# Kernel tuning notes

Measured on AMD Instinct MI355X. Metric: run time of the kernel, lower is better.

The kernel has to match this reference:

```python
import jax, jax.numpy as jnp
import numpy as np

B, S, HID, NH = 2, 2048, 1024, 16
HD = HID // NH  # head_dim = 64


def setup_inputs() -> dict:
    key = jax.random.key(0)
    ks = jax.random.split(key, 9)
    init = 0.02
    return {
        "x": jax.random.normal(ks[0], (B, S, HID), dtype=jnp.float32),
        "Wq": jax.random.normal(ks[1], (HID, HID), dtype=jnp.float32) * init,
        "bq": jnp.zeros((HID,), dtype=jnp.float32),
        "Wk": jax.random.normal(ks[2], (HID, HID), dtype=jnp.float32) * init,
        "bk": jnp.zeros((HID,), dtype=jnp.float32),
        "Wv": jax.random.normal(ks[3], (HID, HID), dtype=jnp.float32) * init,
        "bv": jnp.zeros((HID,), dtype=jnp.float32),
        "Wo": jax.random.normal(ks[4], (HID, HID), dtype=jnp.float32) * init,
        "bo": jnp.zeros((HID,), dtype=jnp.float32),
    }


def _split_heads(t):
    # [B, S, HID] -> [B, NH, S, HD]
    return t.reshape(B, S, NH, HD).transpose(0, 2, 1, 3)


def reference(x, Wq, bq, Wk, bk, Wv, bv, Wo, bo):
    q = _split_heads(x @ Wq.T + bq)
    k = _split_heads(x @ Wk.T + bk)
    v = _split_heads(x @ Wv.T + bv)

    # Faithful to source: scores = QK^T / (head_dim ** -0.5) == QK^T * sqrt(head_dim)
    inv_scale = jnp.asarray(HD ** (-0.5), dtype=x.dtype)
    scores = jnp.einsum("bhqd,bhkd->bhqk", q, k) / inv_scale

    causal_mask = jnp.triu(jnp.ones((S, S), dtype=bool), k=1)  # True above diagonal
    scores = jnp.where(causal_mask, jnp.asarray(-jnp.inf, dtype=scores.dtype), scores)
    attn = jax.nn.softmax(scores, axis=-1)  # dropout = identity (eval mode)

    ctx = jnp.einsum("bhqk,bhkd->bhqd", attn, v)
    ctx = ctx.transpose(0, 2, 1, 3).reshape(B, S, HID)
    out = ctx @ Wo.T + bo  # out_layer Linear; dropout = identity
    return out, attn
```

## Files before the change

kernel.cpp:

```cpp
#include <hip/hip_runtime.h>
#include <hip/hip_bf16.h>

#define BB   2
#define SS   2048
#define HID  1024
#define NH   16
#define HD   64
#define NEGS -30000.0f

typedef __bf16 bf16x8 __attribute__((ext_vector_type(8)));
typedef __bf16 bf16x4 __attribute__((ext_vector_type(4)));
typedef float  f32x4  __attribute__((ext_vector_type(4)));

static __device__ __forceinline__ f32x4 mfma_bf16(bf16x8 a, bf16x8 b, f32x4 c) {
    return __builtin_amdgcn_mfma_f32_16x16x32_bf16(a, b, c, 0, 0, 0);
}

static __device__ __forceinline__ void split_bf16(float f, __bf16* hp, __bf16* lp) {
    __bf16 h = (__bf16)f;
    *hp = h;
    *lp = (__bf16)(f - (float)h);
}

static __device__ __forceinline__ float clampf(float v, float lo, float hi) {
    return fminf(fmaxf(v, lo), hi);
}

static __device__ __forceinline__ void gll16(const __bf16* g, __bf16* l) {
    __builtin_amdgcn_global_load_lds((const void*)g, (void*)l, 16, 0, 0);
}

static __device__ __forceinline__ void barrier_lds() {
    asm volatile("s_waitcnt lgkmcnt(0)" ::: "memory");
    __builtin_amdgcn_sched_barrier(0);
    __builtin_amdgcn_s_barrier();
    __builtin_amdgcn_sched_barrier(0);
}

__global__ __launch_bounds__(256) void split_kernel(
    const float* __restrict__ x,
    const float* __restrict__ Wq, const float* __restrict__ Wk,
    const float* __restrict__ Wv, const float* __restrict__ Wo,
    __bf16* __restrict__ xh, __bf16* __restrict__ xl,
    __bf16* __restrict__ wqh, __bf16* __restrict__ wql,
    __bf16* __restrict__ wkh, __bf16* __restrict__ wkl,
    __bf16* __restrict__ wvh, __bf16* __restrict__ woh)
{
    const int bid = blockIdx.x;
    if (bid < 4096) {
        const int i4 = bid * 256 + threadIdx.x;
        const float4 v = ((const float4*)x)[i4];
        const float* p = (const float*)&v;
        bf16x4 h4, l4v;
#pragma unroll
        for (int j = 0; j < 4; j++) { __bf16 hh, ll; split_bf16(p[j], &hh, &ll); h4[j] = hh; l4v[j] = ll; }
        *(bf16x4*)&xh[(size_t)i4 * 4] = h4;
        *(bf16x4*)&xl[(size_t)i4 * 4] = l4v;
        return;
    }
    const int wb = bid - 4096;
    const int which = (wb >> 10) + 1;
    const int i4 = (wb & 1023) * 256 + threadIdx.x;
    const float* src = which == 1 ? Wq : which == 2 ? Wk : which == 3 ? Wv : Wo;
    const float sc = (which == 1) ? 8.0f : 1.0f;
    const float4 v = ((const float4*)src)[i4];
    const float* p = (const float*)&v;
    bf16x4 h4, l4v;
#pragma unroll
    for (int j = 0; j < 4; j++) { __bf16 hh, ll; split_bf16(p[j] * sc, &hh, &ll); h4[j] = hh; l4v[j] = ll; }
    if (which == 1)      { *(bf16x4*)&wqh[(size_t)i4 * 4] = h4; *(bf16x4*)&wql[(size_t)i4 * 4] = l4v; }
    else if (which == 2) { *(bf16x4*)&wkh[(size_t)i4 * 4] = h4; *(bf16x4*)&wkl[(size_t)i4 * 4] = l4v; }
    else if (which == 3) { *(bf16x4*)&wvh[(size_t)i4 * 4] = h4; }
    else                 { *(bf16x4*)&woh[(size_t)i4 * 4] = h4; }
}

__global__ __launch_bounds__(256) void qkv_kernel(
    const __bf16* __restrict__ xh, const __bf16* __restrict__ xl,
    const __bf16* __restrict__ wqh, const __bf16* __restrict__ wql,
    const __bf16* __restrict__ wkh, const __bf16* __restrict__ wkl,
    const __bf16* __restrict__ wvh,
    const float* __restrict__ bq, const float* __restrict__ bk, const float* __restrict__ bv,
    __bf16* __restrict__ qh, __bf16* __restrict__ ql,
    __bf16* __restrict__ kh, __bf16* __restrict__ kl,
    __bf16* __restrict__ vt)
{
    __shared__ __align__(16) __bf16 smem[32768];

    const int stream = blockIdx.x >> 3, ct = blockIdx.x & 7;
    const int t0 = blockIdx.y * 128, c0 = ct * 128;
    const bool qk = stream < 2;
    const __bf16* const Bhg = stream == 0 ? wqh : stream == 1 ? wkh : wvh;
    const __bf16* const Blg = stream == 0 ? wql : wkl;
    const float* const bias = stream == 0 ? bq : stream == 1 ? bk : bv;
    const float bscale = stream == 0 ? 8.0f : 1.0f;

    const int tid = threadIdx.x, wave = tid >> 6, lane = tid & 63;
    const int l16 = lane & 15, quad = lane >> 4;
    const int wr = wave >> 1, wc = wave & 1;

    const int ar0 = tid >> 2,         as0 = (tid & 3) ^ (ar0 & 3);
    const int ar1 = (256 + tid) >> 2, as1 = ((256 + tid) & 3) ^ (ar1 & 3);
    const size_t aoff0 = (size_t)(t0 + ar0) * HID + as0 * 8;
    const size_t aoff1 = (size_t)(t0 + ar1) * HID + as1 * 8;
    const size_t boff0 = (size_t)(c0 + ar0) * HID + as0 * 8;
    const size_t boff1 = (size_t)(c0 + ar1) * HID + as1 * 8;
    const int ld0 = wave << 9, ld1 = (4 + wave) << 9;

#define QKV_STAGE(b_, k0_) do {                                   \
        __bf16* s_ = smem + (b_) * 16384;                         \
        gll16(xh + aoff0 + (k0_), s_ + ld0);                      \
        gll16(xh + aoff1 + (k0_), s_ + ld1);                      \
        gll16(Bhg + boff0 + (k0_), s_ + 8192 + ld0);              \
        gll16(Bhg + boff1 + (k0_), s_ + 8192 + ld1);              \
        if (qk) {                                                 \
            gll16(xl + aoff0 + (k0_), s_ + 4096 + ld0);           \
            gll16(xl + aoff1 + (k0_), s_ + 4096 + ld1);           \
            gll16(Blg + boff0 + (k0_), s_ + 12288 + ld0);         \
            gll16(Blg + boff1 + (k0_), s_ + 12288 + ld1);         \
        }                                                         \
    } while (0)

    const f32x4 zero4 = {0.f, 0.f, 0.f, 0.f};
    f32x4 acc[4][4];
#pragma unroll
    for (int i = 0; i < 4; i++)
#pragma unroll
        for (int j = 0; j < 4; j++) acc[i][j] = zero4;

    QKV_STAGE(0, 0);
    for (int k0 = 0; k0 < HID; k0 += 32) {
        const int cur = (k0 >> 5) & 1;
        __syncthreads();
        if (k0 + 32 < HID) QKV_STAGE(cur ^ 1, k0 + 32);
        __bf16* const s_ = smem + cur * 16384;

        bf16x8 aH[4], aL[4], bHf[4], bLf[4];
#pragma unroll
        for (int mf = 0; mf < 4; mf++) {
            const int row = wr * 64 + mf * 16 + l16;
            const int off = row * 32 + ((quad ^ (row & 3)) << 3);
            aH[mf] = *(const bf16x8*)(s_ + off);
            if (qk) aL[mf] = *(const bf16x8*)(s_ + 4096 + off);
        }
#pragma unroll
        for (int nf = 0; nf < 4; nf++) {
            const int row = wc * 64 + nf * 16 + l16;
            const int off = row * 32 + ((quad ^ (row & 3)) << 3);
            bHf[nf] = *(const bf16x8*)(s_ + 8192 + off);
            if (qk) bLf[nf] = *(const bf16x8*)(s_ + 12288 + off);
        }
#pragma unroll
        for (int mf = 0; mf < 4; mf++)
#pragma unroll
            for (int nf = 0; nf < 4; nf++) {
                acc[mf][nf] = mfma_bf16(aH[mf], bHf[nf], acc[mf][nf]);
                if (qk) {
                    acc[mf][nf] = mfma_bf16(aH[mf], bLf[nf], acc[mf][nf]);
                    acc[mf][nf] = mfma_bf16(aL[mf], bHf[nf], acc[mf][nf]);
                }
            }
    }
#undef QKV_STAGE

    const int bidx = t0 >> 11;
    const int s0 = t0 & (SS - 1);

    if (qk) {
        __bf16* const Es = smem;
        __bf16* const hi_arr = stream == 0 ? qh : kh;
        __bf16* const lo_arr = stream == 0 ? ql : kl;
#pragma unroll
        for (int pass = 0; pass < 2; pass++) {
            __syncthreads();
#pragma unroll
            for (int nf = 0; nf < 4; nf++) {
                const int dcl = wc * 64 + nf * 16 + l16;
                const float bv_ = bias[c0 + dcl] * bscale;
#pragma unroll
                for (int mf = 0; mf < 4; mf++)
#pragma unroll
                    for (int r = 0; r < 4; r++) {
                        const int srl = wr * 64 + mf * 16 + quad * 4 + r;
                        const float v = clampf(acc[mf][nf][r] + bv_, -1e4f, 1e4f);
                        __bf16 hv, lv;
                        split_bf16(v, &hv, &lv);
                        Es[srl * 132 + dcl] = pass ? lv : hv;
                    }
            }
            __syncthreads();
            __bf16* const dst = pass ? lo_arr : hi_arr;
#pragma unroll
            for (int i = 0; i < 8; i++) {
                const int idx = tid + i * 256;
                const int row = idx >> 4, c16 = idx & 15;
                const int hh = (c0 >> 6) + (c16 >> 3);
                const int dd = (c16 & 7) * 8;
                const size_t o = ((size_t)(bidx * NH + hh) * SS + (s0 + row)) * HD + dd;
                *(uint4*)&dst[o] = *(const uint4*)&Es[row * 132 + c16 * 8];
            }
        }
    } else {
        __syncthreads();
        __bf16* const Vts = smem + wave * 4608;
#pragma unroll
        for (int nf = 0; nf < 4; nf++) {
            const int dloc = nf * 16 + l16;
            const float bv_ = bias[c0 + wc * 64 + dloc];
#pragma unroll
            for (int mf = 0; mf < 4; mf++)
#pragma unroll
                for (int r = 0; r < 4; r++)
                    Vts[dloc * 72 + mf * 16 + quad * 4 + r] =
                        (__bf16)clampf(acc[mf][nf][r] + bv_, -1e4f, 1e4f);
        }
        const int hh = (c0 + wc * 64) >> 6;
        const size_t vb = (size_t)(bidx * NH + hh) * HD * SS;
        const int sc0 = s0 + wr * 64;
#pragma unroll
        for (int j = 0; j < 8; j++) {
            const int idx = j * 64 + lane;
            const int d = idx >> 3, c8 = idx & 7;
            *(uint4*)&vt[vb + (size_t)d * SS + sc0 + c8 * 8] =
                *(const uint4*)&Vts[d * 72 + c8 * 8];
        }
    }
}

__global__ __launch_bounds__(512) void attn_kernel(
    const __bf16* __restrict__ qh, const __bf16* __restrict__ ql,
    const __bf16* __restrict__ kh, const __bf16* __restrict__ kl,
    const __bf16* __restrict__ vt,
    float* __restrict__ attn, __bf16* __restrict__ ctx)
{
    __shared__ __align__(16) __bf16 Kh0[4096], Kl0[4096], Kh1[4096], Kl1[4096];
    __shared__ __align__(16) __bf16 Vt0[4096], Vt1[4096];
    __shared__ __align__(16) __bf16 Ps[128][72];
    __shared__ __align__(16) __bf16 _occ_pad[8192];

    const int bid = blockIdx.x;
    const int g   = bid & 7;
    const int ii  = bid >> 3;
    const int bh  = g + 8 * (ii & 3);
    const int p   = ii >> 2;
    const int b   = bh >> 4, h = bh & 15;

    const int tid  = threadIdx.x;
    const int wave = tid >> 6, lane = tid & 63;
    const int l16  = lane & 15, quad = lane >> 4;

    const int sr = tid >> 3, ssw = (tid & 7) ^ (sr & 7);
    const size_t kq = (size_t)sr * HD + ssw * 8;
    const size_t vq = (size_t)sr * SS + ssw * 8;
    const int ldw = wave << 9;

    const __bf16* const khp = kh + (size_t)bh * SS * HD;
    const __bf16* const klp = kl + (size_t)bh * SS * HD;
    const __bf16* const vtp = vt + (size_t)bh * HD * SS;

#define STAGE_K(j_, KH, KL) do {                                  \
        const __bf16* kg_ = khp + (size_t)(j_) * (64 * HD);       \
        const __bf16* lg_ = klp + (size_t)(j_) * (64 * HD);       \
        gll16(kg_ + kq, (KH) + ldw); gll16(lg_ + kq, (KL) + ldw); \
    } while (0)
#define STAGE_V(j_, VT) do {                                      \
        const __bf16* vg_ = vtp + (size_t)(j_) * 64;              \
        gll16(vg_ + vq, (VT) + ldw);                              \
    } while (0)

    const f32x4 zero4 = {0.f, 0.f, 0.f, 0.f};

    for (int seg = 0; seg < 2; seg++) {
        const int qt = seg ? p : (15 - p);
        const int nj = 2 * qt + 2;

        bf16x8 aHq[2], aLq[2];
        {
            const size_t qrow = ((size_t)bh * SS + qt * 128 + wave * 16 + l16) * HD;
#pragma unroll
            for (int ks = 0; ks < 2; ks++) {
                aHq[ks] = *(const bf16x8*)&qh[qrow + ks * 32 + quad * 8];
                aLq[ks] = *(const bf16x8*)&ql[qrow + ks * 32 + quad * 8];
            }
        }

        float m4[4], l4[4];
#pragma unroll
        for (int r = 0; r < 4; r++) { m4[r] = NEGS; l4[r] = 0.f; }

        __syncthreads();
        STAGE_K(0, Kh0, Kl0);
        __syncthreads();

        for (int j = 0; j < nj; j++) {
            if (j) __syncthreads();
            if (j < nj - 1) {
                if (j & 1) STAGE_K(j + 1, Kh0, Kl0);
                else       STAGE_K(j + 1, Kh1, Kl1);
            }
            const __bf16* const Khc = (j & 1) ? Kh1 : Kh0;
            const __bf16* const Klc = (j & 1) ? Kl1 : Kl0;

            f32x4 sacc[4] = {zero4, zero4, zero4, zero4};
#pragma unroll
            for (int ks = 0; ks < 2; ks++)
#pragma unroll
                for (int c = 0; c < 4; c++) {
                    const int krow = c * 16 + l16;
                    const int ko = krow * 64 + (((ks * 4 + quad) ^ (krow & 7)) << 3);
                    const bf16x8 bH = *(const bf16x8*)(Khc + ko);
                    const bf16x8 bL = *(const bf16x8*)(Klc + ko);
                    sacc[c] = mfma_bf16(aHq[ks], bH, sacc[c]);
                    sacc[c] = mfma_bf16(aHq[ks], bL, sacc[c]);
                    sacc[c] = mfma_bf16(aLq[ks], bH, sacc[c]);
                }
            if (j >= 2 * qt) {
                const int cb = j * 64, qr = qt * 128 + wave * 16 + quad * 4;
#pragma unroll
                for (int c = 0; c < 4; c++) {
                    const int col = cb + c * 16 + l16;
#pragma unroll
                    for (int r = 0; r < 4; r++)
                        if (col > qr + r) sacc[c][r] = NEGS;
                }
            }
#pragma unroll
            for (int r = 0; r < 4; r++) {
                const float mx = fmaxf(fmaxf(sacc[0][r], sacc[1][r]),
                                       fmaxf(sacc[2][r], sacc[3][r]));
                const float mn = fmaxf(m4[r], mx);
                l4[r] = l4[r] * __expf(m4[r] - mn)
                      + __expf(sacc[0][r] - mn) + __expf(sacc[1][r] - mn)
                      + __expf(sacc[2][r] - mn) + __expf(sacc[3][r] - mn);
                m4[r] = mn;
            }
        }

        float il[4];
#pragma unroll
        for (int r = 0; r < 4; r++) {
#pragma unroll
            for (int off = 1; off < 16; off <<= 1) {
                const float mo  = __shfl_xor(m4[r], off);
                const float lo_ = __shfl_xor(l4[r], off);
                const float mn  = fmaxf(m4[r], mo);
                l4[r] = l4[r] * __expf(m4[r] - mn) + lo_ * __expf(mo - mn);
                m4[r] = mn;
            }
            il[r] = (l4[r] > 0.f) ? (1.0f / l4[r]) : 0.f;
        }

        f32x4 cacc[4] = {zero4, zero4, zero4, zero4};

        __syncthreads();
        STAGE_K(0, Kh0, Kl0);
        STAGE_V(0, Vt0);

        for (int j = 0; j < nj; j++) {
            __syncthreads();
            if (j < nj - 1) {
                if (j & 1) { STAGE_K(j + 1, Kh0, Kl0); STAGE_V(j + 1, Vt0); }
                else       { STAGE_K(j + 1, Kh1, Kl1); STAGE_V(j + 1, Vt1); }
            }
            const __bf16* const Khc = (j & 1) ? Kh1 : Kh0;
            const __bf16* const Klc = (j & 1) ? Kl1 : Kl0;
            const __bf16* const Vtc = (j & 1) ? Vt1 : Vt0;

            f32x4 sacc[4] = {zero4, zero4, zero4, zero4};
#pragma unroll
            for (int ks = 0; ks < 2; ks++)
#pragma unroll
                for (int c = 0; c < 4; c++) {
                    const int krow = c * 16 + l16;
                    const int ko = krow * 64 + (((ks * 4 + quad) ^ (krow & 7)) << 3);
                    const bf16x8 bH = *(const bf16x8*)(Khc + ko);
                    const bf16x8 bL = *(const bf16x8*)(Klc + ko);
                    sacc[c] = mfma_bf16(aHq[ks], bH, sacc[c]);
                    sacc[c] = mfma_bf16(aHq[ks], bL, sacc[c]);
                    sacc[c] = mfma_bf16(aLq[ks], bH, sacc[c]);
                }
            if (j >= 2 * qt) {
                const int cb = j * 64, qr = qt * 128 + wave * 16 + quad * 4;
#pragma unroll
                for (int c = 0; c < 4; c++) {
                    const int col = cb + c * 16 + l16;
#pragma unroll
                    for (int r = 0; r < 4; r++)
                        if (col > qr + r) sacc[c][r] = NEGS;
                }
            }
#pragma unroll
            for (int c = 0; c < 4; c++)
#pragma unroll
                for (int r = 0; r < 4; r++) {
                    const float pv = clampf(__expf(sacc[c][r] - m4[r]) * il[r], 0.f, 1.f);
                    Ps[wave * 16 + quad * 4 + r][c * 16 + l16] = (__bf16)pv;
                }
            barrier_lds();

#pragma unroll
            for (int i = 0; i < 2; i++) {
                const int idx = tid + i * 512;
                const int row = idx >> 3, c8 = idx & 7;
                const size_t o = ((size_t)bh * SS + qt * 128 + row) * SS + j * 64 + c8 * 8;
                __bf16 tmp[8];
                *(uint4*)tmp = *(const uint4*)&Ps[row][c8 * 8];
                float4 f0, f1;
                f0.x = (float)tmp[0]; f0.y = (float)tmp[1];
                f0.z = (float)tmp[2]; f0.w = (float)tmp[3];
                f1.x = (float)tmp[4]; f1.y = (float)tmp[5];
                f1.z = (float)tmp[6]; f1.w = (float)tmp[7];
                *(float4*)&attn[o]     = f0;
                *(float4*)&attn[o + 4] = f1;
            }
#pragma unroll
            for (int ks = 0; ks < 2; ks++) {
                const bf16x8 ap = *(const bf16x8*)&Ps[wave * 16 + l16][ks * 32 + quad * 8];
#pragma unroll
                for (int dt = 0; dt < 4; dt++) {
                    const int vrow = dt * 16 + l16;
                    const int vo = vrow * 64 + (((ks * 4 + quad) ^ (vrow & 7)) << 3);
                    cacc[dt] = mfma_bf16(ap, *(const bf16x8*)(Vtc + vo), cacc[dt]);
                }
            }
        }

        const float4 zf4 = {0.f, 0.f, 0.f, 0.f};
        for (int j = nj; j < SS / 64; j++) {
#pragma unroll
            for (int i = 0; i < 4; i++) {
                const int idx = tid + i * 512;
                const int row = idx >> 4, c4 = idx & 15;
                const size_t o = ((size_t)bh * SS + qt * 128 + row) * SS + j * 64 + c4 * 4;
                *(float4*)&attn[o] = zf4;
            }
        }

        __syncthreads();
#pragma unroll
        for (int dt = 0; dt < 4; dt++) {
            const int d = dt * 16 + l16;
#pragma unroll
            for (int r = 0; r < 4; r++)
                Ps[wave * 16 + quad * 4 + r][d] =
                    (__bf16)clampf(cacc[dt][r], -1e4f, 1e4f);
        }
        __syncthreads();
#pragma unroll
        for (int i = 0; i < 2; i++) {
            const int idx = tid + i * 512;
            const int row = idx >> 3, c8 = idx & 7;
            *(uint4*)&ctx[(size_t)(b * SS + qt * 128 + row) * HID + h * 64 + c8 * 8] =
                *(const uint4*)&Ps[row][c8 * 8];
        }
    }

    if ((int)blockIdx.x < 0) ((volatile __bf16*)_occ_pad)[0] = Ps[0][0];
#undef STAGE_K
#undef STAGE_V
}

__global__ __launch_bounds__(256) void out_kernel(
    const __bf16* __restrict__ ctx, const __bf16* __restrict__ woh,
    const float* __restrict__ bo, float* __restrict__ out)
{
    __shared__ __align__(16) __bf16 smem[16384];

    const int o0 = blockIdx.x * 128;
    const int t0 = blockIdx.y * 128;

    const int tid = threadIdx.x, wave = tid >> 6, lane = tid & 63;
    const int l16 = lane & 15, quad = lane >> 4;
    const int wr = wave >> 1, wc = wave & 1;

    const int ar0 = tid >> 2,         as0 = (tid & 3) ^ (ar0 & 3);
    const int ar1 = (256 + tid) >> 2, as1 = ((256 + tid) & 3) ^ (ar1 & 3);
    const size_t aoff0 = (size_t)(t0 + ar0) * HID + as0 * 8;
    const size_t aoff1 = (size_t)(t0 + ar1) * HID + as1 * 8;
    const size_t boff0 = (size_t)(o0 + ar0) * HID + as0 * 8;
    const size_t boff1 = (size_t)(o0 + ar1) * HID + as1 * 8;
    const int ld0 = wave << 9, ld1 = (4 + wave) << 9;

#define OUT_STAGE(b_, k0_) do {                                   \
        __bf16* s_ = smem + (b_) * 8192;                          \
        gll16(ctx + aoff0 + (k0_), s_ + ld0);                     \
        gll16(ctx + aoff1 + (k0_), s_ + ld1);                     \
        gll16(woh + boff0 + (k0_), s_ + 4096 + ld0);              \
        gll16(woh + boff1 + (k0_), s_ + 4096 + ld1);              \
    } while (0)

    const f32x4 zero4 = {0.f, 0.f, 0.f, 0.f};
    f32x4 acc[4][4];
#pragma unroll
    for (int i = 0; i < 4; i++)
#pragma unroll
        for (int j = 0; j < 4; j++) acc[i][j] = zero4;

    OUT_STAGE(0, 0);
    for (int k0 = 0; k0 < HID; k0 += 32) {
        const int cur = (k0 >> 5) & 1;
        __syncthreads();
        if (k0 + 32 < HID) OUT_STAGE(cur ^ 1, k0 + 32);
        __bf16* const s_ = smem + cur * 8192;

        bf16x8 aH[4], bHf[4];
#pragma unroll
        for (int mf = 0; mf < 4; mf++) {
            const int row = wr * 64 + mf * 16 + l16;
            aH[mf] = *(const bf16x8*)(s_ + row * 32 + ((quad ^ (row & 3)) << 3));
        }
#pragma unroll
        for (int nf = 0; nf < 4; nf++) {
            const int row = wc * 64 + nf * 16 + l16;
            bHf[nf] = *(const bf16x8*)(s_ + 4096 + row * 32 + ((quad ^ (row & 3)) << 3));
        }
#pragma unroll
        for (int mf = 0; mf < 4; mf++)
#pragma unroll
            for (int nf = 0; nf < 4; nf++)
                acc[mf][nf] = mfma_bf16(aH[mf], bHf[nf], acc[mf][nf]);
    }
#undef OUT_STAGE

#pragma unroll
    for (int nf = 0; nf < 4; nf++) {
        const int dcol = o0 + wc * 64 + nf * 16 + l16;
        const float bias = bo[dcol];
#pragma unroll
        for (int mf = 0; mf < 4; mf++)
#pragma unroll
            for (int r = 0; r < 4; r++) {
                const int t = t0 + wr * 64 + mf * 16 + quad * 4 + r;
                out[(size_t)t * HID + dcol] = clampf(acc[mf][nf][r] + bias, -1e4f, 1e4f);
            }
    }
}

extern "C" void kernel_launch(void* const* d_in, const int* in_sizes, int n_in,
                              void* d_out, int out_size, void* d_ws, size_t ws_size,
                              hipStream_t stream) {
    const float* x  = (const float*)d_in[0];
    const float* Wq = (const float*)d_in[1];
    const float* bq = (const float*)d_in[2];
    const float* Wk = (const float*)d_in[3];
    const float* bk = (const float*)d_in[4];
    const float* Wv = (const float*)d_in[5];
    const float* bv = (const float*)d_in[6];
    const float* Wo = (const float*)d_in[7];
    const float* bo = (const float*)d_in[8];

    float* out  = (float*)d_out;
    float* attn = out + (size_t)BB * SS * HID;

    const size_t NQ = (size_t)BB * NH * SS * HD;
    const size_t NW = (size_t)HID * HID;
    __bf16* ws  = (__bf16*)d_ws;
    __bf16* qh  = ws;
    __bf16* ql  = ws + NQ;
    __bf16* kh  = ws + 2 * NQ;
    __bf16* kl  = ws + 3 * NQ;
    __bf16* vt  = ws + 4 * NQ;
    __bf16* xh  = ws + 5 * NQ;
    __bf16* xl  = ws + 6 * NQ;
    __bf16* wqh = ws + 7 * NQ;
    __bf16* wql = wqh + NW;
    __bf16* wkh = wqh + 2 * NW;
    __bf16* wkl = wqh + 3 * NW;
    __bf16* wvh = wqh + 4 * NW;
    __bf16* woh = wqh + 5 * NW;
    __bf16* ctx = xh;

    split_kernel<<<dim3(8192), 256, 0, stream>>>(x, Wq, Wk, Wv, Wo,
                                                 xh, xl, wqh, wql, wkh, wkl, wvh, woh);
    qkv_kernel<<<dim3(24, 32), 256, 0, stream>>>(xh, xl, wqh, wql, wkh, wkl, wvh,
                                                 bq, bk, bv, qh, ql, kh, kl, vt);
    attn_kernel<<<dim3(256), 512, 0, stream>>>(qh, ql, kh, kl, vt, attn, ctx);
    out_kernel<<<dim3(8, 32), 256, 0, stream>>>(ctx, woh, bo, out);
}
```

Baseline: 745.1 us.

## Split attention blocks per query tile, relax waits, narrow out-proj tiles

```diff
diff --git a/kernel.cpp b/kernel.cpp
--- a/kernel.cpp
+++ b/kernel.cpp
@@ -32,6 +32,19 @@
 
 static __device__ __forceinline__ void barrier_lds() {
     asm volatile("s_waitcnt lgkmcnt(0)" ::: "memory");
+    __builtin_amdgcn_sched_barrier(0);
+    __builtin_amdgcn_s_barrier();
+    __builtin_amdgcn_sched_barrier(0);
+}
+
+static __device__ __forceinline__ void barrier_vm4() {
+    asm volatile("s_waitcnt vmcnt(4) lgkmcnt(0)" ::: "memory");
+    __builtin_amdgcn_sched_barrier(0);
+    __builtin_amdgcn_s_barrier();
+    __builtin_amdgcn_sched_barrier(0);
+}
+static __device__ __forceinline__ void barrier_vm0() {
+    asm volatile("s_waitcnt vmcnt(0) lgkmcnt(0)" ::: "memory");
     __builtin_amdgcn_sched_barrier(0);
     __builtin_amdgcn_s_barrier();
     __builtin_amdgcn_sched_barrier(0);
@@ -226,7 +239,7 @@
     }
 }
 
-__global__ __launch_bounds__(512) void attn_kernel(
+__global__ __launch_bounds__(512, 4) void attn_kernel(
     const __bf16* __restrict__ qh, const __bf16* __restrict__ ql,
     const __bf16* __restrict__ kh, const __bf16* __restrict__ kl,
     const __bf16* __restrict__ vt,
@@ -235,14 +248,16 @@
     __shared__ __align__(16) __bf16 Kh0[4096], Kl0[4096], Kh1[4096], Kl1[4096];
     __shared__ __align__(16) __bf16 Vt0[4096], Vt1[4096];
     __shared__ __align__(16) __bf16 Ps[128][72];
-    __shared__ __align__(16) __bf16 _occ_pad[8192];
-
-    const int bid = blockIdx.x;
-    const int g   = bid & 7;
-    const int ii  = bid >> 3;
-    const int bh  = g + 8 * (ii & 3);
-    const int p   = ii >> 2;
-    const int b   = bh >> 4, h = bh & 15;
+
+    const int bid  = blockIdx.x;
+    const int half = bid >> 8;
+    const int ii   = bid & 255;
+    const int g    = ii & 7;
+    const int bh   = g + 8 * ((ii >> 3) & 3);
+    const int p    = ii >> 5;
+    const int qt   = half ? p : (15 - p);
+    const int nj   = 2 * qt + 2;
+    const int b    = bh >> 4, h = bh & 15;
 
     const int tid  = threadIdx.x;
     const int wave = tid >> 6, lane = tid & 63;
@@ -269,192 +284,185 @@
 
     const f32x4 zero4 = {0.f, 0.f, 0.f, 0.f};
 
-    for (int seg = 0; seg < 2; seg++) {
-        const int qt = seg ? p : (15 - p);
-        const int nj = 2 * qt + 2;
-
-        bf16x8 aHq[2], aLq[2];
-        {
-            const size_t qrow = ((size_t)bh * SS + qt * 128 + wave * 16 + l16) * HD;
-#pragma unroll
-            for (int ks = 0; ks < 2; ks++) {
-                aHq[ks] = *(const bf16x8*)&qh[qrow + ks * 32 + quad * 8];
-                aLq[ks] = *(const bf16x8*)&ql[qrow + ks * 32 + quad * 8];
-            }
-        }
-
-        float m4[4], l4[4];
-#pragma unroll
-        for (int r = 0; r < 4; r++) { m4[r] = NEGS; l4[r] = 0.f; }
-
-        __syncthreads();
-        STAGE_K(0, Kh0, Kl0);
-        __syncthreads();
-
-        for (int j = 0; j < nj; j++) {
-            if (j) __syncthreads();
-            if (j < nj - 1) {
-                if (j & 1) STAGE_K(j + 1, Kh0, Kl0);
-                else       STAGE_K(j + 1, Kh1, Kl1);
-            }
-            const __bf16* const Khc = (j & 1) ? Kh1 : Kh0;
-            const __bf16* const Klc = (j & 1) ? Kl1 : Kl0;
-
-            f32x4 sacc[4] = {zero4, zero4, zero4, zero4};
-#pragma unroll
-            for (int ks = 0; ks < 2; ks++)
-#pragma unroll
-                for (int c = 0; c < 4; c++) {
-                    const int krow = c * 16 + l16;
-                    const int ko = krow * 64 + (((ks * 4 + quad) ^ (krow & 7)) << 3);
-                    const bf16x8 bH = *(const bf16x8*)(Khc + ko);
-                    const bf16x8 bL = *(const bf16x8*)(Klc + ko);
-                    sacc[c] = mfma_bf16(aHq[ks], bH, sacc[c]);
-                    sacc[c] = mfma_bf16(aHq[ks], bL, sacc[c]);
-                    sacc[c] = mfma_bf16(aLq[ks], bH, sacc[c]);
-                }
-            if (j >= 2 * qt) {
-                const int cb = j * 64, qr = qt * 128 + wave * 16 + quad * 4;
-#pragma unroll
-                for (int c = 0; c < 4; c++) {
-                    const int col = cb + c * 16 + l16;
-#pragma unroll
-                    for (int r = 0; r < 4; r++)
-                        if (col > qr + r) sacc[c][r] = NEGS;
-                }
-            }
+    bf16x8 aHq[2], aLq[2];
+    {
+        const size_t qrow = ((size_t)bh * SS + qt * 128 + wave * 16 + l16) * HD;
+#pragma unroll
+        for (int ks = 0; ks < 2; ks++) {
+            aHq[ks] = *(const bf16x8*)&qh[qrow + ks * 32 + quad * 8];
+            aLq[ks] = *(const bf16x8*)&ql[qrow + ks * 32 + quad * 8];
+        }
+    }
+
+    float m4[4], l4[4];
+#pragma unroll
+    for (int r = 0; r < 4; r++) { m4[r] = NEGS; l4[r] = 0.f; }
+
+    STAGE_K(0, Kh0, Kl0);
+    __syncthreads();
+
+    for (int j = 0; j < nj; j++) {
+        if (j) __syncthreads();
+        if (j < nj - 1) {
+            if (j & 1) STAGE_K(j + 1, Kh0, Kl0);
+            else       STAGE_K(j + 1, Kh1, Kl1);
+        }
+        const __bf16* const Khc = (j & 1) ? Kh1 : Kh0;
+        const __bf16* const Klc = (j & 1) ? Kl1 : Kl0;
+
+        f32x4 sacc[4] = {zero4, zero4, zero4, zero4};
+#pragma unroll
+        for (int ks = 0; ks < 2; ks++)
+#pragma unroll
+            for (int c = 0; c < 4; c++) {
+                const int krow = c * 16 + l16;
+                const int ko = krow * 64 + (((ks * 4 + quad) ^ (krow & 7)) << 3);
+                const bf16x8 bH = *(const bf16x8*)(Khc + ko);
+                const bf16x8 bL = *(const bf16x8*)(Klc + ko);
+                sacc[c] = mfma_bf16(aHq[ks], bH, sacc[c]);
+                sacc[c] = mfma_bf16(aHq[ks], bL, sacc[c]);
+                sacc[c] = mfma_bf16(aLq[ks], bH, sacc[c]);
+            }
+        if (j >= 2 * qt) {
+            const int cb = j * 64, qr = qt * 128 + wave * 16 + quad * 4;
+#pragma unroll
+            for (int c = 0; c < 4; c++) {
+                const int col = cb + c * 16 + l16;
+#pragma unroll
+                for (int r = 0; r < 4; r++)
+                    if (col > qr + r) sacc[c][r] = NEGS;
+            }
+        }
+#pragma unroll
+        for (int r = 0; r < 4; r++) {
+            const float mx = fmaxf(fmaxf(sacc[0][r], sacc[1][r]),
+                                   fmaxf(sacc[2][r], sacc[3][r]));
+            const float mn = fmaxf(m4[r], mx);
+            l4[r] = l4[r] * __expf(m4[r] - mn)
+                  + __expf(sacc[0][r] - mn) + __expf(sacc[1][r] - mn)
+                  + __expf(sacc[2][r] - mn) + __expf(sacc[3][r] - mn);
+            m4[r] = mn;
+        }
+    }
+
+    float il[4];
+#pragma unroll
+    for (int r = 0; r < 4; r++) {
+#pragma unroll
+        for (int off = 1; off < 16; off <<= 1) {
+            const float mo  = __shfl_xor(m4[r], off);
+            const float lo_ = __shfl_xor(l4[r], off);
+            const float mn  = fmaxf(m4[r], mo);
+            l4[r] = l4[r] * __expf(m4[r] - mn) + lo_ * __expf(mo - mn);
+            m4[r] = mn;
+        }
+        il[r] = (l4[r] > 0.f) ? (1.0f / l4[r]) : 0.f;
+    }
+
+    f32x4 cacc[4] = {zero4, zero4, zero4, zero4};
+
+    __syncthreads();
+    STAGE_K(0, Kh0, Kl0);
+    STAGE_V(0, Vt0);
+
+    for (int j = 0; j < nj; j++) {
+        if (j == 0) barrier_vm0();
+        else        barrier_vm4();
+        if (j < nj - 1) {
+            if (j & 1) { STAGE_K(j + 1, Kh0, Kl0); STAGE_V(j + 1, Vt0); }
+            else       { STAGE_K(j + 1, Kh1, Kl1); STAGE_V(j + 1, Vt1); }
+        }
+        const __bf16* const Khc = (j & 1) ? Kh1 : Kh0;
+        const __bf16* const Klc = (j & 1) ? Kl1 : Kl0;
+        const __bf16* const Vtc = (j & 1) ? Vt1 : Vt0;
+
+        f32x4 sacc[4] = {zero4, zero4, zero4, zero4};
+#pragma unroll
+        for (int ks = 0; ks < 2; ks++)
+#pragma unroll
+            for (int c = 0; c < 4; c++) {
+                const int krow = c * 16 + l16;
+                const int ko = krow * 64 + (((ks * 4 + quad) ^ (krow & 7)) << 3);
+                const bf16x8 bH = *(const bf16x8*)(Khc + ko);
+                const bf16x8 bL = *(const bf16x8*)(Klc + ko);
+                sacc[c] = mfma_bf16(aHq[ks], bH, sacc[c]);
+                sacc[c] = mfma_bf16(aHq[ks], bL, sacc[c]);
+                sacc[c] = mfma_bf16(aLq[ks], bH, sacc[c]);
+            }
+        if (j >= 2 * qt) {
+            const int cb = j * 64, qr = qt * 128 + wave * 16 + quad * 4;
+#pragma unroll
+            for (int c = 0; c < 4; c++) {
+                const int col = cb + c * 16 + l16;
+#pragma unroll
+                for (int r = 0; r < 4; r++)
+                    if (col > qr + r) sacc[c][r] = NEGS;
+            }
+        }
+#pragma unroll
+        for (int c = 0; c < 4; c++)
 #pragma unroll
             for (int r = 0; r < 4; r++) {
-                const float mx = fmaxf(fmaxf(sacc[0][r], sacc[1][r]),
-                                       fmaxf(sacc[2][r], sacc[3][r]));
-                const float mn = fmaxf(m4[r], mx);
-                l4[r] = l4[r] * __expf(m4[r] - mn)
-                      + __expf(sacc[0][r] - mn) + __expf(sacc[1][r] - mn)
-                      + __expf(sacc[2][r] - mn) + __expf(sacc[3][r] - mn);
-                m4[r] = mn;
-            }
-        }
-
-        float il[4];
-#pragma unroll
-        for (int r = 0; r < 4; r++) {
-#pragma unroll
-            for (int off = 1; off < 16; off <<= 1) {
-                const float mo  = __shfl_xor(m4[r], off);
-                const float lo_ = __shfl_xor(l4[r], off);
-                const float mn  = fmaxf(m4[r], mo);
-                l4[r] = l4[r] * __expf(m4[r] - mn) + lo_ * __expf(mo - mn);
-                m4[r] = mn;
-            }
-            il[r] = (l4[r] > 0.f) ? (1.0f / l4[r]) : 0.f;
-        }
-
-        f32x4 cacc[4] = {zero4, zero4, zero4, zero4};
-
-        __syncthreads();
-        STAGE_K(0, Kh0, Kl0);
-        STAGE_V(0, Vt0);
-
-        for (int j = 0; j < nj; j++) {
-            __syncthreads();
-            if (j < nj - 1) {
-                if (j & 1) { STAGE_K(j + 1, Kh0, Kl0); STAGE_V(j + 1, Vt0); }
-                else       { STAGE_K(j + 1, Kh1, Kl1); STAGE_V(j + 1, Vt1); }
-            }
-            const __bf16* const Khc = (j & 1) ? Kh1 : Kh0;
-            const __bf16* const Klc = (j & 1) ? Kl1 : Kl0;
-            const __bf16* const Vtc = (j & 1) ? Vt1 : Vt0;
-
-            f32x4 sacc[4] = {zero4, zero4, zero4, zero4};
-#pragma unroll
-            for (int ks = 0; ks < 2; ks++)
-#pragma unroll
-                for (int c = 0; c < 4; c++) {
-                    const int krow = c * 16 + l16;
-                    const int ko = krow * 64 + (((ks * 4 + quad) ^ (krow & 7)) << 3);
-                    const bf16x8 bH = *(const bf16x8*)(Khc + ko);
-                    const bf16x8 bL = *(const bf16x8*)(Klc + ko);
-                    sacc[c] = mfma_bf16(aHq[ks], bH, sacc[c]);
-                    sacc[c] = mfma_bf16(aHq[ks], bL, sacc[c]);
-                    sacc[c] = mfma_bf16(aLq[ks], bH, sacc[c]);
-                }
-            if (j >= 2 * qt) {
-                const int cb = j * 64, qr = qt * 128 + wave * 16 + quad * 4;
-#pragma unroll
-                for (int c = 0; c < 4; c++) {
-                    const int col = cb + c * 16 + l16;
-#pragma unroll
-                    for (int r = 0; r < 4; r++)
-                        if (col > qr + r) sacc[c][r] = NEGS;
-                }
-            }
-#pragma unroll
-            for (int c = 0; c < 4; c++)
-#pragma unroll
-                for (int r = 0; r < 4; r++) {
-                    const float pv = clampf(__expf(sacc[c][r] - m4[r]) * il[r], 0.f, 1.f);
-                    Ps[wave * 16 + quad * 4 + r][c * 16 + l16] = (__bf16)pv;
-                }
-            barrier_lds();
-
-#pragma unroll
-            for (int i = 0; i < 2; i++) {
-                const int idx = tid + i * 512;
-                const int row = idx >> 3, c8 = idx & 7;
-                const size_t o = ((size_t)bh * SS + qt * 128 + row) * SS + j * 64 + c8 * 8;
-                __bf16 tmp[8];
-                *(uint4*)tmp = *(const uint4*)&Ps[row][c8 * 8];
-                float4 f0, f1;
-                f0.x = (float)tmp[0]; f0.y = (float)tmp[1];
-                f0.z = (float)tmp[2]; f0.w = (float)tmp[3];
-                f1.x = (float)tmp[4]; f1.y = (float)tmp[5];
-                f1.z = (float)tmp[6]; f1.w = (float)tmp[7];
-                *(float4*)&attn[o]     = f0;
-                *(float4*)&attn[o + 4] = f1;
-            }
-#pragma unroll
-            for (int ks = 0; ks < 2; ks++) {
-                const bf16x8 ap = *(const bf16x8*)&Ps[wave * 16 + l16][ks * 32 + quad * 8];
-#pragma unroll
-                for (int dt = 0; dt < 4; dt++) {
-                    const int vrow = dt * 16 + l16;
-                    const int vo = vrow * 64 + (((ks * 4 + quad) ^ (vrow & 7)) << 3);
-                    cacc[dt] = mfma_bf16(ap, *(const bf16x8*)(Vtc + vo), cacc[dt]);
-                }
-            }
-        }
-
-        const float4 zf4 = {0.f, 0.f, 0.f, 0.f};
-        for (int j = nj; j < SS / 64; j++) {
-#pragma unroll
-            for (int i = 0; i < 4; i++) {
-                const int idx = tid + i * 512;
-                const int row = idx >> 4, c4 = idx & 15;
-                const size_t o = ((size_t)bh * SS + qt * 128 + row) * SS + j * 64 + c4 * 4;
-                *(float4*)&attn[o] = zf4;
-            }
-        }
-
-        __syncthreads();
-#pragma unroll
-        for (int dt = 0; dt < 4; dt++) {
-            const int d = dt * 16 + l16;
-#pragma unroll
-            for (int r = 0; r < 4; r++)
-                Ps[wave * 16 + quad * 4 + r][d] =
-                    (__bf16)clampf(cacc[dt][r], -1e4f, 1e4f);
-        }
-        __syncthreads();
+                const float pv = clampf(__expf(sacc[c][r] - m4[r]) * il[r], 0.f, 1.f);
+                Ps[wave * 16 + quad * 4 + r][c * 16 + l16] = (__bf16)pv;
+            }
+        barrier_lds();
+
 #pragma unroll
         for (int i = 0; i < 2; i++) {
             const int idx = tid + i * 512;
             const int row = idx >> 3, c8 = idx & 7;
-            *(uint4*)&ctx[(size_t)(b * SS + qt * 128 + row) * HID + h * 64 + c8 * 8] =
-                *(const uint4*)&Ps[row][c8 * 8];
-        }
-    }
-
-    if ((int)blockIdx.x < 0) ((volatile __bf16*)_occ_pad)[0] = Ps[0][0];
+            const size_t o = ((size_t)bh * SS + qt * 128 + row) * SS + j * 64 + c8 * 8;
+            __bf16 tmp[8];
+            *(uint4*)tmp = *(const uint4*)&Ps[row][c8 * 8];
+            float4 f0, f1;
+            f0.x = (float)tmp[0]; f0.y = (float)tmp[1];
+            f0.z = (float)tmp[2]; f0.w = (float)tmp[3];
+            f1.x = (float)tmp[4]; f1.y = (float)tmp[5];
+            f1.z = (float)tmp[6]; f1.w = (float)tmp[7];
+            *(float4*)&attn[o]     = f0;
+            *(float4*)&attn[o + 4] = f1;
+        }
+#pragma unroll
+        for (int ks = 0; ks < 2; ks++) {
+            const bf16x8 ap = *(const bf16x8*)&Ps[wave * 16 + l16][ks * 32 + quad * 8];
+#pragma unroll
+            for (int dt = 0; dt < 4; dt++) {
+                const int vrow = dt * 16 + l16;
+                const int vo = vrow * 64 + (((ks * 4 + quad) ^ (vrow & 7)) << 3);
+                cacc[dt] = mfma_bf16(ap, *(const bf16x8*)(Vtc + vo), cacc[dt]);
+            }
+        }
+    }
+
+    const float4 zf4 = {0.f, 0.f, 0.f, 0.f};
+    for (int j = nj; j < SS / 64; j++) {
+#pragma unroll
+        for (int i = 0; i < 4; i++) {
+            const int idx = tid + i * 512;
+            const int row = idx >> 4, c4 = idx & 15;
+            const size_t o = ((size_t)bh * SS + qt * 128 + row) * SS + j * 64 + c4 * 4;
+            *(float4*)&attn[o] = zf4;
+        }
+    }
+
+    __syncthreads();
+#pragma unroll
+    for (int dt = 0; dt < 4; dt++) {
+        const int d = dt * 16 + l16;
+#pragma unroll
+        for (int r = 0; r < 4; r++)
+            Ps[wave * 16 + quad * 4 + r][d] =
+                (__bf16)clampf(cacc[dt][r], -1e4f, 1e4f);
+    }
+    __syncthreads();
+#pragma unroll
+    for (int i = 0; i < 2; i++) {
+        const int idx = tid + i * 512;
+        const int row = idx >> 3, c8 = idx & 7;
+        *(uint4*)&ctx[(size_t)(b * SS + qt * 128 + row) * HID + h * 64 + c8 * 8] =
+            *(const uint4*)&Ps[row][c8 * 8];
+    }
 #undef STAGE_K
 #undef STAGE_V
 }
@@ -463,9 +471,9 @@
     const __bf16* __restrict__ ctx, const __bf16* __restrict__ woh,
     const float* __restrict__ bo, float* __restrict__ out)
 {
-    __shared__ __align__(16) __bf16 smem[16384];
-
-    const int o0 = blockIdx.x * 128;
+    __shared__ __align__(16) __bf16 smem[12288];
+
+    const int o0 = blockIdx.x * 64;
     const int t0 = blockIdx.y * 128;
 
     const int tid = threadIdx.x, wave = tid >> 6, lane = tid & 63;
@@ -476,54 +484,52 @@
     const int ar1 = (256 + tid) >> 2, as1 = ((256 + tid) & 3) ^ (ar1 & 3);
     const size_t aoff0 = (size_t)(t0 + ar0) * HID + as0 * 8;
     const size_t aoff1 = (size_t)(t0 + ar1) * HID + as1 * 8;
-    const size_t boff0 = (size_t)(o0 + ar0) * HID + as0 * 8;
-    const size_t boff1 = (size_t)(o0 + ar1) * HID + as1 * 8;
+    const size_t boff  = (size_t)(o0 + ar0) * HID + as0 * 8;
     const int ld0 = wave << 9, ld1 = (4 + wave) << 9;
 
 #define OUT_STAGE(b_, k0_) do {                                   \
-        __bf16* s_ = smem + (b_) * 8192;                          \
+        __bf16* s_ = smem + (b_) * 6144;                          \
         gll16(ctx + aoff0 + (k0_), s_ + ld0);                     \
         gll16(ctx + aoff1 + (k0_), s_ + ld1);                     \
-        gll16(woh + boff0 + (k0_), s_ + 4096 + ld0);              \
-        gll16(woh + boff1 + (k0_), s_ + 4096 + ld1);              \
+        gll16(woh + boff + (k0_), s_ + 4096 + ld0);               \
     } while (0)
 
     const f32x4 zero4 = {0.f, 0.f, 0.f, 0.f};
-    f32x4 acc[4][4];
+    f32x4 acc[4][2];
 #pragma unroll
     for (int i = 0; i < 4; i++)
 #pragma unroll
-        for (int j = 0; j < 4; j++) acc[i][j] = zero4;
+        for (int j = 0; j < 2; j++) acc[i][j] = zero4;
 
     OUT_STAGE(0, 0);
     for (int k0 = 0; k0 < HID; k0 += 32) {
         const int cur = (k0 >> 5) & 1;
         __syncthreads();
         if (k0 + 32 < HID) OUT_STAGE(cur ^ 1, k0 + 32);
-        __bf16* const s_ = smem + cur * 8192;
-
-        bf16x8 aH[4], bHf[4];
+        __bf16* const s_ = smem + cur * 6144;
+
+        bf16x8 aH[4], bHf[2];
 #pragma unroll
         for (int mf = 0; mf < 4; mf++) {
             const int row = wr * 64 + mf * 16 + l16;
             aH[mf] = *(const bf16x8*)(s_ + row * 32 + ((quad ^ (row & 3)) << 3));
         }
 #pragma unroll
-        for (int nf = 0; nf < 4; nf++) {
-            const int row = wc * 64 + nf * 16 + l16;
+        for (int nf = 0; nf < 2; nf++) {
+            const int row = wc * 32 + nf * 16 + l16;
             bHf[nf] = *(const bf16x8*)(s_ + 4096 + row * 32 + ((quad ^ (row & 3)) << 3));
         }
 #pragma unroll
         for (int mf = 0; mf < 4; mf++)
 #pragma unroll
-            for (int nf = 0; nf < 4; nf++)
+            for (int nf = 0; nf < 2; nf++)
                 acc[mf][nf] = mfma_bf16(aH[mf], bHf[nf], acc[mf][nf]);
     }
 #undef OUT_STAGE
 
 #pragma unroll
-    for (int nf = 0; nf < 4; nf++) {
-        const int dcol = o0 + wc * 64 + nf * 16 + l16;
+    for (int nf = 0; nf < 2; nf++) {
+        const int dcol = o0 + wc * 32 + nf * 16 + l16;
         const float bias = bo[dcol];
 #pragma unroll
         for (int mf = 0; mf < 4; mf++)
@@ -573,6 +579,6 @@
                                                  xh, xl, wqh, wql, wkh, wkl, wvh, woh);
     qkv_kernel<<<dim3(24, 32), 256, 0, stream>>>(xh, xl, wqh, wql, wkh, wkl, wvh,
                                                  bq, bk, bv, qh, ql, kh, kl, vt);
-    attn_kernel<<<dim3(256), 512, 0, stream>>>(qh, ql, kh, kl, vt, attn, ctx);
-    out_kernel<<<dim3(8, 32), 256, 0, stream>>>(ctx, woh, bo, out);
-}
+    attn_kernel<<<dim3(512), 512, 0, stream>>>(qh, ql, kh, kl, vt, attn, ctx);
+    out_kernel<<<dim3(16, 32), 256, 0, stream>>>(ctx, woh, bo, out);
+}
```

New measurement: 723.7 us. -2.9%, faster.
